# Kernel optimization log

Hardware: AMD Instinct MI355X
Metric: run time of the kernel (lower is better)

Reference implementation:

```python
import jax, jax.numpy as jnp
import numpy as np

NUM_USERS = 80000
NUM_ITEMS = 40000
NUM_NODES = NUM_USERS + NUM_ITEMS
LATENT_DIM = 64
N_LAYERS = 3
ALPHA = 0.8
E_POS = 3_000_000
E_NEG = 1_500_000
E_PATH = 2_000_000
N_PATHS = 6


def _make_edges(rng, n_edges, n_nodes):
    # sample keys, dedupe so COO is coalesced (distinct (row,col) pairs)
    keys = rng.integers(0, n_nodes * n_nodes, size=int(n_edges * 1.05), dtype=np.int64)
    keys = np.unique(keys)[:n_edges]
    assert keys.shape[0] == n_edges
    row = (keys // n_nodes).astype(np.int32)
    col = (keys % n_nodes).astype(np.int32)
    return row, col


def setup_inputs() -> dict:
    key = jax.random.key(0)
    k1, k2, k3, k4, k5 = jax.random.split(key, 5)
    rng = np.random.default_rng(0)

    pos_row, pos_col = _make_edges(rng, E_POS, NUM_NODES)
    neg_row, neg_col = _make_edges(rng, E_NEG, NUM_NODES)
    p_row, p_col = _make_edges(rng, E_PATH, NUM_NODES)

    # path membership counts: for each coalesced edge, how many times each of the
    # 6 path matrices contains it (0/1 here); at least one path per edge
    counts = (rng.random((E_PATH, N_PATHS)) < 0.5).astype(np.float32)
    empty = counts.sum(axis=1) == 0
    counts[empty, 0] = 1.0

    return {
        "user_emb": 0.1 * jax.random.normal(k1, (NUM_USERS, LATENT_DIM), jnp.float32),
        "item_emb": 0.1 * jax.random.normal(k2, (NUM_ITEMS, LATENT_DIM), jnp.float32),
        "theta": jnp.ones((N_PATHS,), jnp.float32) / N_PATHS,
        "pos_row": jnp.asarray(pos_row),
        "pos_col": jnp.asarray(pos_col),
        "pos_val": jax.random.uniform(k3, (E_POS,), jnp.float32, 0.01, 1.0),
        "neg_row": jnp.asarray(neg_row),
        "neg_col": jnp.asarray(neg_col),
        "neg_val": jax.random.uniform(k4, (E_NEG,), jnp.float32, 0.01, 1.0),
        "p_row": jnp.asarray(p_row),
        "p_col": jnp.asarray(p_col),
        "p_counts": jnp.asarray(counts),
    }


def _spmm(row, col, val, x, n_nodes):
    # y = A @ x with A given as COO edge list: gather + segment scatter-add
    return jax.ops.segment_sum(val[:, None] * x[col], row, num_segments=n_nodes)


def reference(user_emb, item_emb, theta, pos_row, pos_col, pos_val,
              neg_row, neg_col, neg_val, p_row, p_col, p_counts):
    n = NUM_NODES

    # ---- build path-weighted matrix (coalesce + sparse row softmax, eq.(2)) ----
    theta_w = jax.nn.softmax(theta)                 # [6]
    vals = p_counts @ theta_w                       # coalesced values per edge [E_path]
    exp_v = jnp.exp(vals)
    row_sums = jax.ops.segment_sum(exp_v, p_row, num_segments=n)
    soft_v = exp_v / (row_sums[p_row] + 1e-12)      # row-level sparse softmax

    # ---- PEE: E_0 = P @ all_emb ----
    all_emb = jnp.concatenate([user_emb, item_emb], axis=0)  # [N, D]
    e = _spmm(p_row, p_col, soft_v, all_emb, n)
    embs = [e]

    # ---- signed propagation ----
    for _ in range(N_LAYERS):
        e_pos = _spmm(pos_row, pos_col, pos_val, e, n)
        e_neg_a = _spmm(neg_row, neg_col, neg_val, e, n)
        e = e_pos + ALPHA * (e - e_neg_a)
        embs.append(e)

    light_out = jnp.mean(jnp.stack(embs, axis=1), axis=1)   # [N, D]
    users = light_out[:NUM_USERS]
    items = light_out[NUM_USERS:]
    return users, items
```

## Files before the change

### kernel.cpp

```cpp
#include <hip/hip_runtime.h>

#define NUM_USERS 80000
#define NUM_ITEMS 40000
#define NUM_NODES 120000
#define DIM 64
#define ALPHA_C 0.8f

typedef unsigned short u16;
typedef unsigned int u32;

__device__ __forceinline__ u16 f2bf(float f) {
    union { float f; u32 i; } v;
    v.f = f;
    u32 i = v.i;
    u32 r = (i + 0x7FFFu + ((i >> 16) & 1u)) >> 16;
    return (u16)r;
}
__device__ __forceinline__ float lo_bf(u32 u) { return __uint_as_float(u << 16); }
__device__ __forceinline__ float hi_bf(u32 u) { return __uint_as_float(u & 0xffff0000u); }

__device__ __forceinline__ void acc8(float* __restrict__ acc, float v, uint4 q) {
    const u32* p = (const u32*)&q;
#pragma unroll
    for (int k = 0; k < 4; ++k) {
        u32 u = p[k];
        acc[2 * k]     = fmaf(v, lo_bf(u), acc[2 * k]);
        acc[2 * k + 1] = fmaf(v, hi_bf(u), acc[2 * k + 1]);
    }
}

__global__ void k_softmax_theta(const float* __restrict__ theta,
                                float* __restrict__ theta_w) {
    if (threadIdx.x == 0 && blockIdx.x == 0) {
        float m = -1e30f;
        for (int i = 0; i < 6; ++i) m = fmaxf(m, theta[i]);
        float e[6];
        float s = 0.f;
        for (int i = 0; i < 6; ++i) { e[i] = expf(theta[i] - m); s += e[i]; }
        for (int i = 0; i < 6; ++i) theta_w[i] = e[i] / s;
    }
}

__global__ void k_expv(const float* __restrict__ p_counts,
                       const float* __restrict__ theta_w,
                       float* __restrict__ exp_v, int E) {
    int i = blockIdx.x * blockDim.x + threadIdx.x;
    if (i >= E) return;
    const float* c = p_counts + (size_t)i * 6;
    float v = c[0] * theta_w[0] + c[1] * theta_w[1] + c[2] * theta_w[2] +
              c[3] * theta_w[3] + c[4] * theta_w[4] + c[5] * theta_w[5];
    exp_v[i] = expf(v);
}

__device__ __forceinline__ void lower_bound_ptr(const int* __restrict__ rows,
                                                int nnz, int r,
                                                int* __restrict__ ptr) {
    int lo = 0, hi = nnz;
    while (lo < hi) {
        int mid = (lo + hi) >> 1;
        if (rows[mid] < r) lo = mid + 1; else hi = mid;
    }
    ptr[r] = lo;
}

__global__ void k_row_ptr3(const int* __restrict__ rows_a, int nnz_a, int* __restrict__ pa,
                           const int* __restrict__ rows_b, int nnz_b, int* __restrict__ pb,
                           const int* __restrict__ rows_c, int nnz_c, int* __restrict__ pc) {
    int t = blockIdx.x * blockDim.x + threadIdx.x;
    int which = t / (NUM_NODES + 1);
    int r = t - which * (NUM_NODES + 1);
    if (which == 0) lower_bound_ptr(rows_a, nnz_a, r, pa);
    else if (which == 1) lower_bound_ptr(rows_b, nnz_b, r, pb);
    else if (which == 2) lower_bound_ptr(rows_c, nnz_c, r, pc);
}

__global__ void k_cvt(const float* __restrict__ user_emb,
                      const float* __restrict__ item_emb,
                      u16* __restrict__ emb16) {
    int i = blockIdx.x * blockDim.x + threadIdx.x;
    size_t f = (size_t)i * 4;
    const size_t UTOT = (size_t)NUM_USERS * DIM;
    const size_t TOT = (size_t)NUM_NODES * DIM;
    if (f >= TOT) return;
    float4 v = (f < UTOT) ? *(const float4*)(user_emb + f)
                          : *(const float4*)(item_emb + (f - UTOT));
    ushort4 o;
    o.x = f2bf(v.x); o.y = f2bf(v.y); o.z = f2bf(v.z); o.w = f2bf(v.w);
    *(ushort4*)(emb16 + f) = o;
}

__device__ __forceinline__ void seg_gather_nr(const int* __restrict__ col,
                                              const float* __restrict__ val,
                                              int start, int end,
                                              const u16* __restrict__ x,
                                              int group, int li,
                                              float* __restrict__ acc) {
    int e = start + group;
    for (; e + 8 < end; e += 16) {
        int c0 = col[e];
        float v0 = val[e];
        int c1 = col[e + 8];
        float v1 = val[e + 8];
        uint4 x0 = *((const uint4*)(x + (size_t)c0 * DIM) + li);
        uint4 x1 = *((const uint4*)(x + (size_t)c1 * DIM) + li);
        acc8(acc, v0, x0);
        acc8(acc, v1, x1);
    }
    if (e < end) {
        int c0 = col[e];
        float v0 = val[e];
        uint4 x0 = *((const uint4*)(x + (size_t)c0 * DIM) + li);
        acc8(acc, v0, x0);
    }
}

__device__ __forceinline__ void reduce8(float* __restrict__ acc) {
#pragma unroll
    for (int m = 8; m < 64; m <<= 1) {
#pragma unroll
        for (int k = 0; k < 8; ++k) acc[k] += __shfl_xor(acc[k], m);
    }
}

__global__ void k_path(const u16* __restrict__ emb16,
                       const float* __restrict__ exp_v,
                       const int* __restrict__ rp,
                       const int* __restrict__ cols,
                       u16* __restrict__ e0,
                       float* __restrict__ sum_out) {
    int wid = (blockIdx.x * blockDim.x + threadIdx.x) >> 6;
    if (wid >= NUM_NODES) return;
    int lane = threadIdx.x & 63;
    int group = lane >> 3, li = lane & 7;
    int start = rp[wid], end = rp[wid + 1];

    float s = 0.f;
    for (int e = start + lane; e < end; e += 64) s += exp_v[e];
#pragma unroll
    for (int m = 1; m < 64; m <<= 1) s += __shfl_xor(s, m);
    float inv = 1.0f / (s + 1e-12f);

    float acc[8];
#pragma unroll
    for (int k = 0; k < 8; ++k) acc[k] = 0.f;

    int e = start + group;
    for (; e + 8 < end; e += 16) {
        int c0 = cols[e];
        float w0 = exp_v[e] * inv;
        int c1 = cols[e + 8];
        float w1 = exp_v[e + 8] * inv;
        uint4 x0 = *((const uint4*)(emb16 + (size_t)c0 * DIM) + li);
        uint4 x1 = *((const uint4*)(emb16 + (size_t)c1 * DIM) + li);
        acc8(acc, w0, x0);
        acc8(acc, w1, x1);
    }
    if (e < end) {
        int c0 = cols[e];
        float w0 = exp_v[e] * inv;
        uint4 x0 = *((const uint4*)(emb16 + (size_t)c0 * DIM) + li);
        acc8(acc, w0, x0);
    }
    reduce8(acc);

    if (lane < 8) {
        u32 o[4];
#pragma unroll
        for (int k = 0; k < 4; ++k)
            o[k] = (u32)f2bf(acc[2 * k]) | ((u32)f2bf(acc[2 * k + 1]) << 16);
        *((uint4*)(e0 + (size_t)wid * DIM) + li) = *(uint4*)o;
        float4* sp = (float4*)(sum_out + (size_t)wid * DIM) + li * 2;
        sp[0] = make_float4(acc[0], acc[1], acc[2], acc[3]);
        sp[1] = make_float4(acc[4], acc[5], acc[6], acc[7]);
    }
}

__global__ void k_layer(const u16* __restrict__ e_in,
                        u16* __restrict__ e_out,
                        float* __restrict__ sum_io,
                        const int* __restrict__ rp_p,
                        const int* __restrict__ col_p,
                        const float* __restrict__ val_p,
                        const int* __restrict__ rp_n,
                        const int* __restrict__ col_n,
                        const float* __restrict__ val_n,
                        int is_final) {
    int wid = (blockIdx.x * blockDim.x + threadIdx.x) >> 6;
    if (wid >= NUM_NODES) return;
    int lane = threadIdx.x & 63;
    int group = lane >> 3, li = lane & 7;

    float accp[8], accn[8];
#pragma unroll
    for (int k = 0; k < 8; ++k) { accp[k] = 0.f; accn[k] = 0.f; }

    seg_gather_nr(col_p, val_p, rp_p[wid], rp_p[wid + 1], e_in, group, li, accp);
    seg_gather_nr(col_n, val_n, rp_n[wid], rp_n[wid + 1], e_in, group, li, accn);
    reduce8(accp);
    reduce8(accn);

    if (lane < 8) {
        uint4 eq = *((const uint4*)(e_in + (size_t)wid * DIM) + li);
        const u32* ep = (const u32*)&eq;
        float res[8];
#pragma unroll
        for (int k = 0; k < 4; ++k) {
            res[2 * k]     = accp[2 * k]     + ALPHA_C * (lo_bf(ep[k]) - accn[2 * k]);
            res[2 * k + 1] = accp[2 * k + 1] + ALPHA_C * (hi_bf(ep[k]) - accn[2 * k + 1]);
        }
        float4* sp = (float4*)(sum_io + (size_t)wid * DIM) + li * 2;
        float4 s0 = sp[0], s1 = sp[1];
        s0.x += res[0]; s0.y += res[1]; s0.z += res[2]; s0.w += res[3];
        s1.x += res[4]; s1.y += res[5]; s1.z += res[6]; s1.w += res[7];
        if (is_final) {
            s0.x *= 0.25f; s0.y *= 0.25f; s0.z *= 0.25f; s0.w *= 0.25f;
            s1.x *= 0.25f; s1.y *= 0.25f; s1.z *= 0.25f; s1.w *= 0.25f;
        }
        sp[0] = s0; sp[1] = s1;
        if (!is_final) {
            u32 o[4];
#pragma unroll
            for (int k = 0; k < 4; ++k)
                o[k] = (u32)f2bf(res[2 * k]) | ((u32)f2bf(res[2 * k + 1]) << 16);
            *((uint4*)(e_out + (size_t)wid * DIM) + li) = *(uint4*)o;
        }
    }
}

extern "C" void kernel_launch(void* const* d_in, const int* in_sizes, int n_in,
                              void* d_out, int out_size, void* d_ws, size_t ws_size,
                              hipStream_t stream) {
    const float* user_emb = (const float*)d_in[0];
    const float* item_emb = (const float*)d_in[1];
    const float* theta    = (const float*)d_in[2];
    const int*   pos_row  = (const int*)d_in[3];
    const int*   pos_col  = (const int*)d_in[4];
    const float* pos_val  = (const float*)d_in[5];
    const int*   neg_row  = (const int*)d_in[6];
    const int*   neg_col  = (const int*)d_in[7];
    const float* neg_val  = (const float*)d_in[8];
    const int*   p_row    = (const int*)d_in[9];
    const int*   p_col    = (const int*)d_in[10];
    const float* p_counts = (const float*)d_in[11];
    const int E_pos  = in_sizes[3];
    const int E_neg  = in_sizes[6];
    const int E_path = in_sizes[9];

    char* wsb = (char*)d_ws;
    size_t off = 0;
    auto alloc = [&](size_t bytes) -> void* {
        void* p = wsb + off;
        off = (off + bytes + 255) & ~(size_t)255;
        return p;
    };
    float* theta_w = (float*)alloc(6 * sizeof(float));
    float* exp_v   = (float*)alloc((size_t)E_path * sizeof(float));
    int*   rp_pos  = (int*)alloc((size_t)(NUM_NODES + 1) * sizeof(int));
    int*   rp_neg  = (int*)alloc((size_t)(NUM_NODES + 1) * sizeof(int));
    int*   rp_path = (int*)alloc((size_t)(NUM_NODES + 1) * sizeof(int));
    u16*   emb16   = (u16*)alloc((size_t)NUM_NODES * DIM * sizeof(u16));
    u16*   eA      = (u16*)alloc((size_t)NUM_NODES * DIM * sizeof(u16));
    u16*   eB      = (u16*)alloc((size_t)NUM_NODES * DIM * sizeof(u16));
    float* sum_io  = (float*)d_out;

    k_softmax_theta<<<1, 64, 0, stream>>>(theta, theta_w);
    k_expv<<<(E_path + 255) / 256, 256, 0, stream>>>(p_counts, theta_w, exp_v, E_path);

    int total_rp = 3 * (NUM_NODES + 1);
    k_row_ptr3<<<(total_rp + 255) / 256, 256, 0, stream>>>(
        pos_row, E_pos, rp_pos, neg_row, E_neg, rp_neg, p_row, E_path, rp_path);

    int cvt_threads = (NUM_NODES * DIM) / 4;
    k_cvt<<<(cvt_threads + 255) / 256, 256, 0, stream>>>(user_emb, item_emb, emb16);

    int row_blocks = NUM_NODES / 4;

    k_path<<<row_blocks, 256, 0, stream>>>(emb16, exp_v, rp_path, p_col, eA, sum_io);
    k_layer<<<row_blocks, 256, 0, stream>>>(eA, eB, sum_io,
                                            rp_pos, pos_col, pos_val,
                                            rp_neg, neg_col, neg_val, 0);
    k_layer<<<row_blocks, 256, 0, stream>>>(eB, eA, sum_io,
                                            rp_pos, pos_col, pos_val,
                                            rp_neg, neg_col, neg_val, 0);
    k_layer<<<row_blocks, 256, 0, stream>>>(eA, eB, sum_io,
                                            rp_pos, pos_col, pos_val,
                                            rp_neg, neg_col, neg_val, 1);
}
```

Baseline: 546.8 us.

## Map each sparse row to an 8-lane group instead of a full wavefront

New measurement: 497.2 us. 9.1% less time.

```diff
diff --git a/kernel.cpp b/kernel.cpp
--- a/kernel.cpp
+++ b/kernel.cpp
@@ -89,18 +89,18 @@
     *(ushort4*)(emb16 + f) = o;
 }
 
-__device__ __forceinline__ void seg_gather_nr(const int* __restrict__ col,
-                                              const float* __restrict__ val,
-                                              int start, int end,
-                                              const u16* __restrict__ x,
-                                              int group, int li,
-                                              float* __restrict__ acc) {
-    int e = start + group;
-    for (; e + 8 < end; e += 16) {
+__device__ __forceinline__ void seg_gather_grp(const int* __restrict__ col,
+                                               const float* __restrict__ val,
+                                               int start, int end,
+                                               const u16* __restrict__ x,
+                                               int li,
+                                               float* __restrict__ acc) {
+    int e = start;
+    for (; e + 1 < end; e += 2) {
         int c0 = col[e];
         float v0 = val[e];
-        int c1 = col[e + 8];
-        float v1 = val[e + 8];
+        int c1 = col[e + 1];
+        float v1 = val[e + 1];
         uint4 x0 = *((const uint4*)(x + (size_t)c0 * DIM) + li);
         uint4 x1 = *((const uint4*)(x + (size_t)c1 * DIM) + li);
         acc8(acc, v0, x0);
@@ -111,14 +111,6 @@
         float v0 = val[e];
         uint4 x0 = *((const uint4*)(x + (size_t)c0 * DIM) + li);
         acc8(acc, v0, x0);
-    }
-}
-
-__device__ __forceinline__ void reduce8(float* __restrict__ acc) {
-#pragma unroll
-    for (int m = 8; m < 64; m <<= 1) {
-#pragma unroll
-        for (int k = 0; k < 8; ++k) acc[k] += __shfl_xor(acc[k], m);
     }
 }
 
@@ -128,28 +120,29 @@
                        const int* __restrict__ cols,
                        u16* __restrict__ e0,
                        float* __restrict__ sum_out) {
-    int wid = (blockIdx.x * blockDim.x + threadIdx.x) >> 6;
-    if (wid >= NUM_NODES) return;
-    int lane = threadIdx.x & 63;
-    int group = lane >> 3, li = lane & 7;
-    int start = rp[wid], end = rp[wid + 1];
+    int t = blockIdx.x * blockDim.x + threadIdx.x;
+    int row = t >> 3;
+    if (row >= NUM_NODES) return;
+    int li = threadIdx.x & 7;
+    int start = rp[row], end = rp[row + 1];
 
     float s = 0.f;
-    for (int e = start + lane; e < end; e += 64) s += exp_v[e];
-#pragma unroll
-    for (int m = 1; m < 64; m <<= 1) s += __shfl_xor(s, m);
+    for (int e = start + li; e < end; e += 8) s += exp_v[e];
+    s += __shfl_xor(s, 1);
+    s += __shfl_xor(s, 2);
+    s += __shfl_xor(s, 4);
     float inv = 1.0f / (s + 1e-12f);
 
     float acc[8];
 #pragma unroll
     for (int k = 0; k < 8; ++k) acc[k] = 0.f;
 
-    int e = start + group;
-    for (; e + 8 < end; e += 16) {
+    int e = start;
+    for (; e + 1 < end; e += 2) {
         int c0 = cols[e];
         float w0 = exp_v[e] * inv;
-        int c1 = cols[e + 8];
-        float w1 = exp_v[e + 8] * inv;
+        int c1 = cols[e + 1];
+        float w1 = exp_v[e + 1] * inv;
         uint4 x0 = *((const uint4*)(emb16 + (size_t)c0 * DIM) + li);
         uint4 x1 = *((const uint4*)(emb16 + (size_t)c1 * DIM) + li);
         acc8(acc, w0, x0);
@@ -161,18 +154,15 @@
         uint4 x0 = *((const uint4*)(emb16 + (size_t)c0 * DIM) + li);
         acc8(acc, w0, x0);
     }
-    reduce8(acc);
-
-    if (lane < 8) {
-        u32 o[4];
-#pragma unroll
-        for (int k = 0; k < 4; ++k)
-            o[k] = (u32)f2bf(acc[2 * k]) | ((u32)f2bf(acc[2 * k + 1]) << 16);
-        *((uint4*)(e0 + (size_t)wid * DIM) + li) = *(uint4*)o;
-        float4* sp = (float4*)(sum_out + (size_t)wid * DIM) + li * 2;
-        sp[0] = make_float4(acc[0], acc[1], acc[2], acc[3]);
-        sp[1] = make_float4(acc[4], acc[5], acc[6], acc[7]);
-    }
+
+    u32 o[4];
+#pragma unroll
+    for (int k = 0; k < 4; ++k)
+        o[k] = (u32)f2bf(acc[2 * k]) | ((u32)f2bf(acc[2 * k + 1]) << 16);
+    *((uint4*)(e0 + (size_t)row * DIM) + li) = *(uint4*)o;
+    float4* sp = (float4*)(sum_out + (size_t)row * DIM) + li * 2;
+    sp[0] = make_float4(acc[0], acc[1], acc[2], acc[3]);
+    sp[1] = make_float4(acc[4], acc[5], acc[6], acc[7]);
 }
 
 __global__ void k_layer(const u16* __restrict__ e_in,
@@ -185,45 +175,41 @@
                         const int* __restrict__ col_n,
                         const float* __restrict__ val_n,
                         int is_final) {
-    int wid = (blockIdx.x * blockDim.x + threadIdx.x) >> 6;
-    if (wid >= NUM_NODES) return;
-    int lane = threadIdx.x & 63;
-    int group = lane >> 3, li = lane & 7;
+    int t = blockIdx.x * blockDim.x + threadIdx.x;
+    int row = t >> 3;
+    if (row >= NUM_NODES) return;
+    int li = threadIdx.x & 7;
 
     float accp[8], accn[8];
 #pragma unroll
     for (int k = 0; k < 8; ++k) { accp[k] = 0.f; accn[k] = 0.f; }
 
-    seg_gather_nr(col_p, val_p, rp_p[wid], rp_p[wid + 1], e_in, group, li, accp);
-    seg_gather_nr(col_n, val_n, rp_n[wid], rp_n[wid + 1], e_in, group, li, accn);
-    reduce8(accp);
-    reduce8(accn);
-
-    if (lane < 8) {
-        uint4 eq = *((const uint4*)(e_in + (size_t)wid * DIM) + li);
-        const u32* ep = (const u32*)&eq;
-        float res[8];
-#pragma unroll
-        for (int k = 0; k < 4; ++k) {
-            res[2 * k]     = accp[2 * k]     + ALPHA_C * (lo_bf(ep[k]) - accn[2 * k]);
-            res[2 * k + 1] = accp[2 * k + 1] + ALPHA_C * (hi_bf(ep[k]) - accn[2 * k + 1]);
-        }
-        float4* sp = (float4*)(sum_io + (size_t)wid * DIM) + li * 2;
-        float4 s0 = sp[0], s1 = sp[1];
-        s0.x += res[0]; s0.y += res[1]; s0.z += res[2]; s0.w += res[3];
-        s1.x += res[4]; s1.y += res[5]; s1.z += res[6]; s1.w += res[7];
-        if (is_final) {
-            s0.x *= 0.25f; s0.y *= 0.25f; s0.z *= 0.25f; s0.w *= 0.25f;
-            s1.x *= 0.25f; s1.y *= 0.25f; s1.z *= 0.25f; s1.w *= 0.25f;
-        }
-        sp[0] = s0; sp[1] = s1;
-        if (!is_final) {
-            u32 o[4];
-#pragma unroll
-            for (int k = 0; k < 4; ++k)
-                o[k] = (u32)f2bf(res[2 * k]) | ((u32)f2bf(res[2 * k + 1]) << 16);
-            *((uint4*)(e_out + (size_t)wid * DIM) + li) = *(uint4*)o;
-        }
+    seg_gather_grp(col_p, val_p, rp_p[row], rp_p[row + 1], e_in, li, accp);
+    seg_gather_grp(col_n, val_n, rp_n[row], rp_n[row + 1], e_in, li, accn);
+
+    uint4 eq = *((const uint4*)(e_in + (size_t)row * DIM) + li);
+    const u32* ep = (const u32*)&eq;
+    float res[8];
+#pragma unroll
+    for (int k = 0; k < 4; ++k) {
+        res[2 * k]     = accp[2 * k]     + ALPHA_C * (lo_bf(ep[k]) - accn[2 * k]);
+        res[2 * k + 1] = accp[2 * k + 1] + ALPHA_C * (hi_bf(ep[k]) - accn[2 * k + 1]);
+    }
+    float4* sp = (float4*)(sum_io + (size_t)row * DIM) + li * 2;
+    float4 s0 = sp[0], s1 = sp[1];
+    s0.x += res[0]; s0.y += res[1]; s0.z += res[2]; s0.w += res[3];
+    s1.x += res[4]; s1.y += res[5]; s1.z += res[6]; s1.w += res[7];
+    if (is_final) {
+        s0.x *= 0.25f; s0.y *= 0.25f; s0.z *= 0.25f; s0.w *= 0.25f;
+        s1.x *= 0.25f; s1.y *= 0.25f; s1.z *= 0.25f; s1.w *= 0.25f;
+    }
+    sp[0] = s0; sp[1] = s1;
+    if (!is_final) {
+        u32 o[4];
+#pragma unroll
+        for (int k = 0; k < 4; ++k)
+            o[k] = (u32)f2bf(res[2 * k]) | ((u32)f2bf(res[2 * k + 1]) << 16);
+        *((uint4*)(e_out + (size_t)row * DIM) + li) = *(uint4*)o;
     }
 }
 
@@ -273,7 +259,7 @@
     int cvt_threads = (NUM_NODES * DIM) / 4;
     k_cvt<<<(cvt_threads + 255) / 256, 256, 0, stream>>>(user_emb, item_emb, emb16);
 
-    int row_blocks = NUM_NODES / 4;
+    int row_blocks = (NUM_NODES + 31) / 32;
 
     k_path<<<row_blocks, 256, 0, stream>>>(emb16, exp_v, rp_path, p_col, eA, sum_io);
     k_layer<<<row_blocks, 256, 0, stream>>>(eA, eB, sum_io,
```
